# Kernel tuning notes

Measured on AMD Instinct MI355X. Metric: run time of the kernel, lower is better.

Reference implementation:

```python
import jax, jax.numpy as jnp
import numpy as np
import math

S, B, L, D = 4096, 2048, 256, 128  # substructure pool, batch, max substructs/drug, hidden


def setup_inputs() -> dict:
    key = jax.random.key(0)
    ks = jax.random.split(key, 6)
    sub_feat = jax.random.normal(ks[0], (S, D), dtype=jnp.float32)
    sub_index = jax.random.randint(ks[1], (B, L), 0, S)
    # ragged lengths -> padded prefix mask (1.0 = valid substructure)
    lengths = jax.random.randint(ks[2], (B,), 8, L + 1)
    mask = (jnp.arange(L)[None, :] < lengths[:, None]).astype(jnp.float32)
    scale = 1.0 / math.sqrt(D)
    Wq = jax.random.normal(ks[3], (D, D), dtype=jnp.float32) * scale
    Wk = jax.random.normal(ks[4], (D, D), dtype=jnp.float32) * scale
    bq = jnp.zeros((D,), dtype=jnp.float32)
    bk = jnp.zeros((D,), dtype=jnp.float32)
    return {"sub_feat": sub_feat, "mask": mask, "Wq": Wq, "bq": bq,
            "Wk": Wk, "bk": bk, "sub_index": sub_index}


def reference(sub_feat, mask, Wq, bq, Wk, bk, sub_index):
    # per-drug gather of substructure ('expert') features: [B, L, D]
    gathered = sub_feat[sub_index]
    # single-head Q/K projections (V is computed but unused in the original)
    q = gathered @ Wq + bq  # [B, L, D]
    k = gathered @ Wk + bk  # [B, L, D]
    inv_sqrt_d = 1.0 / math.sqrt(D)
    # additive mask: (1 - m) * -10000 broadcast over query dim
    add_mask = (1.0 - mask)[:, None, :] * -10000.0  # [B, 1, L]
    scores = jnp.einsum('bid,bjd->bij', q, k) * inv_sqrt_d + add_mask  # [B, L, L]
    probs = jax.nn.softmax(scores, axis=-1)
    # O[:, 0, 0, :] in the original: head 0, query position 0
    score = probs[:, 0, :]  # [B, L]
    # drug_feat[i] = score[i] @ sub_feat[sub_index[i]]
    drug_embeddings = jnp.einsum('bl,bld->bd', score, gathered)  # [B, D]
    return drug_embeddings
```

## Files before the change

### kernel.cpp

```cpp
#include <hip/hip_runtime.h>

#define DIM 128
#define LEN 256
#define INV_SQRT_D 0.08838834764831845f

#define WS_MT   0
#define WS_C    (DIM * DIM)
#define WS_W2   (DIM * DIM + DIM)
#define WS_BQBK (DIM * DIM + 2 * DIM)

__global__ __launch_bounds__(128) void precompute_kernel(
    const float* __restrict__ Wq, const float* __restrict__ bq,
    const float* __restrict__ Wk, const float* __restrict__ bk,
    float* __restrict__ ws)
{
    const int t = threadIdx.x;
    const int j = blockIdx.x;
    if (j < DIM) {
        __shared__ float wqj[DIM];
        wqj[t] = Wq[j * DIM + t];
        __syncthreads();
        const float4* row = reinterpret_cast<const float4*>(Wk + t * DIM);
        float acc = 0.f;
        #pragma unroll 8
        for (int i = 0; i < DIM / 4; ++i) {
            float4 u = row[i];
            acc = fmaf(u.x, wqj[4*i+0], acc);
            acc = fmaf(u.y, wqj[4*i+1], acc);
            acc = fmaf(u.z, wqj[4*i+2], acc);
            acc = fmaf(u.w, wqj[4*i+3], acc);
        }
        ws[WS_MT + j * DIM + t] = acc;
    } else {
        __shared__ float bqs[DIM], bks[DIM], red[DIM];
        bqs[t] = bq[t]; bks[t] = bk[t];
        __syncthreads();
        const float4* rk = reinterpret_cast<const float4*>(Wk + t * DIM);
        const float4* rq = reinterpret_cast<const float4*>(Wq + t * DIM);
        float accC = 0.f, accW = 0.f;
        #pragma unroll 8
        for (int i = 0; i < DIM / 4; ++i) {
            float4 a  = rk[i];
            float4 b2 = rq[i];
            accC = fmaf(a.x,  bqs[4*i+0], accC);
            accC = fmaf(a.y,  bqs[4*i+1], accC);
            accC = fmaf(a.z,  bqs[4*i+2], accC);
            accC = fmaf(a.w,  bqs[4*i+3], accC);
            accW = fmaf(b2.x, bks[4*i+0], accW);
            accW = fmaf(b2.y, bks[4*i+1], accW);
            accW = fmaf(b2.z, bks[4*i+2], accW);
            accW = fmaf(b2.w, bks[4*i+3], accW);
        }
        ws[WS_C  + t] = accC;
        ws[WS_W2 + t] = accW;
        red[t] = bqs[t] * bks[t];
        __syncthreads();
        if (t == 0) {
            float s = 0.f;
            for (int i = 0; i < DIM; ++i) s += red[i];
            ws[WS_BQBK] = s;
        }
    }
}

__global__ __launch_bounds__(256) void fused_kernel(
    const float* __restrict__ sub_feat, const float* __restrict__ mask,
    const int* __restrict__ sub_index, const float* __restrict__ ws,
    float* __restrict__ out)
{
    const int t    = threadIdx.x;
    const int lane = t & 63;
    const int wv   = t >> 6;
    const int pair = wv >> 1;
    const int rhalf= wv & 1;
    const int b    = blockIdx.x * 2 + pair;
    const int c32  = lane & 31;
    const int h    = lane >> 5;
    const int g    = lane >> 4;
    const int m16  = lane & 15;

    const float* Mt = ws + WS_MT;
    const float* cc = ws + WS_C;
    const float* w2 = ws + WS_W2;

    __shared__ float g0s [4][DIM];
    __shared__ int   idxs[4][DIM];
    __shared__ float bias[4][DIM];
    __shared__ float OW  [4][DIM];
    __shared__ float mzw [4][2];

    float* g0w = g0s[wv];
    int*   idw = idxs[wv];
    float* bw  = bias[wv];

    const int*   ib = sub_index + (size_t)b * LEN + rhalf * DIM;
    const float* mb = mask      + (size_t)b * LEN + rhalf * DIM;

    idw[lane]      = ib[lane];
    idw[lane + 64] = ib[lane + 64];
    bw[lane]       = (1.f - mb[lane])      * (-10000.f);
    bw[lane + 64]  = (1.f - mb[lane + 64]) * (-10000.f);

    const int r0 = sub_index[(size_t)b * LEN];
    const float2 g0p = reinterpret_cast<const float2*>(sub_feat + (size_t)r0 * DIM)[lane];
    g0w[2 * lane]     = g0p.x;
    g0w[2 * lane + 1] = g0p.y;

    float qp = g0p.x * w2[2 * lane] + g0p.y * w2[2 * lane + 1];
    #pragma unroll
    for (int o = 32; o > 0; o >>= 1) qp += __shfl_xor(qp, o);
    const float q0bk = qp + ws[WS_BQBK];

    float4 vacc = make_float4(0.f, 0.f, 0.f, 0.f);
    {
        const int jb = h * 64;
        #pragma unroll 8
        for (int k = 0; k < 64; ++k) {
            const int j = jb + k;
            const float gg = g0w[j];
            const float4 u = reinterpret_cast<const float4*>(Mt + j * DIM)[c32];
            vacc.x = fmaf(gg, u.x, vacc.x);
            vacc.y = fmaf(gg, u.y, vacc.y);
            vacc.z = fmaf(gg, u.z, vacc.z);
            vacc.w = fmaf(gg, u.w, vacc.w);
        }
    }
    vacc.x += __shfl_xor(vacc.x, 32);
    vacc.y += __shfl_xor(vacc.y, 32);
    vacc.z += __shfl_xor(vacc.z, 32);
    vacc.w += __shfl_xor(vacc.w, 32);
    const float4 cv = reinterpret_cast<const float4*>(cc)[c32];
    float4 vt;
    vt.x = vacc.x + cv.x; vt.y = vacc.y + cv.y;
    vt.z = vacc.z + cv.z; vt.w = vacc.w + cv.w;

    float4 vA, vB;
    vA.x = __shfl(vt.x, m16);      vA.y = __shfl(vt.y, m16);
    vA.z = __shfl(vt.z, m16);      vA.w = __shfl(vt.w, m16);
    vB.x = __shfl(vt.x, m16 + 16); vB.y = __shfl(vt.y, m16 + 16);
    vB.z = __shfl(vt.z, m16 + 16); vB.w = __shfl(vt.w, m16 + 16);

    float mx = -1e30f, Zr = 0.f;
    float O0=0.f,O1=0.f,O2=0.f,O3=0.f,O4=0.f,O5=0.f,O6=0.f,O7=0.f;
    #pragma unroll 4
    for (int k = 0; k < 32; ++k) {
        const int jl = 4 * k + g;
        const int ij = idw[jl];
        const float bj = bw[jl];
        const float* rp = sub_feat + (size_t)ij * DIM + 4 * m16;
        const float4 u0 = *reinterpret_cast<const float4*>(rp);
        const float4 u1 = *reinterpret_cast<const float4*>(rp + 64);
        float sd = u0.x*vA.x + u0.y*vA.y + u0.z*vA.z + u0.w*vA.w
                 + u1.x*vB.x + u1.y*vB.y + u1.z*vB.z + u1.w*vB.w;
        sd += __shfl_xor(sd, 1);
        sd += __shfl_xor(sd, 2);
        sd += __shfl_xor(sd, 4);
        sd += __shfl_xor(sd, 8);
        const float s  = (sd + q0bk) * INV_SQRT_D + bj;
        const float mn = fmaxf(mx, s);
        const float sc = __expf(mx - mn);
        const float e  = __expf(s - mn);
        Zr = Zr * sc + e;
        O0 = O0*sc + e*u0.x; O1 = O1*sc + e*u0.y;
        O2 = O2*sc + e*u0.z; O3 = O3*sc + e*u0.w;
        O4 = O4*sc + e*u1.x; O5 = O5*sc + e*u1.y;
        O6 = O6*sc + e*u1.z; O7 = O7*sc + e*u1.w;
        mx = mn;
    }

    #pragma unroll
    for (int msk = 16; msk <= 32; msk <<= 1) {
        const float om = __shfl_xor(mx, msk);
        const float oZ = __shfl_xor(Zr, msk);
        const float M  = fmaxf(mx, om);
        const float a  = __expf(mx - M);
        const float bb = __expf(om - M);
        float p0 = __shfl_xor(O0, msk), p1 = __shfl_xor(O1, msk);
        float p2 = __shfl_xor(O2, msk), p3 = __shfl_xor(O3, msk);
        float p4 = __shfl_xor(O4, msk), p5 = __shfl_xor(O5, msk);
        float p6 = __shfl_xor(O6, msk), p7 = __shfl_xor(O7, msk);
        Zr = a*Zr + bb*oZ;
        O0 = a*O0 + bb*p0; O1 = a*O1 + bb*p1;
        O2 = a*O2 + bb*p2; O3 = a*O3 + bb*p3;
        O4 = a*O4 + bb*p4; O5 = a*O5 + bb*p5;
        O6 = a*O6 + bb*p6; O7 = a*O7 + bb*p7;
        mx = M;
    }

    if (lane < 16) {
        reinterpret_cast<float4*>(&OW[wv][0])[m16]  = make_float4(O0, O1, O2, O3);
        reinterpret_cast<float4*>(&OW[wv][64])[m16] = make_float4(O4, O5, O6, O7);
    }
    if (lane == 0) { mzw[wv][0] = mx; mzw[wv][1] = Zr; }
    __syncthreads();

    {
        const int p = t >> 7;
        const int d = t & (DIM - 1);
        const float mA = mzw[2*p][0],   ZA = mzw[2*p][1];
        const float mB = mzw[2*p+1][0], ZB = mzw[2*p+1][1];
        const float M  = fmaxf(mA, mB);
        const float sA = __expf(mA - M);
        const float sB = __expf(mB - M);
        const float Zt = sA * ZA + sB * ZB;
        const float val = (sA * OW[2*p][d] + sB * OW[2*p+1][d]) / Zt;
        out[((size_t)blockIdx.x * 2 + p) * DIM + d] = val;
    }
}

extern "C" void kernel_launch(void* const* d_in, const int* in_sizes, int n_in,
                              void* d_out, int out_size, void* d_ws, size_t ws_size,
                              hipStream_t stream) {
    const float* sub_feat  = (const float*)d_in[0];
    const float* mask      = (const float*)d_in[1];
    const float* Wq        = (const float*)d_in[2];
    const float* bq        = (const float*)d_in[3];
    const float* Wk        = (const float*)d_in[4];
    const float* bk        = (const float*)d_in[5];
    const int*   sub_index = (const int*)d_in[6];
    float* outp = (float*)d_out;
    float* ws   = (float*)d_ws;

    const int B = in_sizes[6] / LEN;

    precompute_kernel<<<dim3(DIM + 1), dim3(DIM), 0, stream>>>(Wq, bq, Wk, bk, ws);
    fused_kernel<<<dim3(B / 2), dim3(256), 0, stream>>>(sub_feat, mask, sub_index, ws, outp);
}
```

Baseline: 31.40 us.

## Split per-drug query vector into separate kernel and drop online-softmax max tracking

Moves the per-drug projection of the query-0 vector through the folded Wq·Wk^T matrix into its own kernel. That kernel stages the 64KB matrix in shared memory and writes the vectors to workspace, and the attention kernel then just loads them. The online softmax max/rescale is replaced by a plain exp2 accumulation with log2e folded into the scale and the mask bias, which removes the per-step rescale and the max merge. This adds a kernel launch and a workspace round-trip. Without max subtraction, exp could overflow if scores are large, so it relies on the score range staying bounded.

```diff
diff --git a/kernel.cpp b/kernel.cpp
--- a/kernel.cpp
+++ b/kernel.cpp
@@ -3,11 +3,14 @@
 #define DIM 128
 #define LEN 256
 #define INV_SQRT_D 0.08838834764831845f
+#define LOG2E 1.4426950408889634f
+#define SCALE_L2 (INV_SQRT_D * LOG2E)
 
 #define WS_MT   0
 #define WS_C    (DIM * DIM)
 #define WS_W2   (DIM * DIM + DIM)
 #define WS_BQBK (DIM * DIM + 2 * DIM)
+#define WS_VBUF (DIM * DIM + 2 * DIM + 8)
 
 __global__ __launch_bounds__(128) void precompute_kernel(
     const float* __restrict__ Wq, const float* __restrict__ bq,
@@ -63,7 +66,140 @@
     }
 }
 
-__global__ __launch_bounds__(256) void fused_kernel(
+__global__ __launch_bounds__(256) void vcompute_kernel(
+    const float* __restrict__ sub_feat, const int* __restrict__ sub_index,
+    const float* __restrict__ ws, float* __restrict__ vout,
+    float* __restrict__ qout, int B)
+{
+    const int t    = threadIdx.x;
+    const int lane = t & 63;
+    const int wv   = t >> 6;
+
+    __shared__ float MtL[DIM * DIM];
+    __shared__ float g0L[4][DIM];
+
+    const float4* Msrc = reinterpret_cast<const float4*>(ws + WS_MT);
+    float4* Mdst = reinterpret_cast<float4*>(MtL);
+    #pragma unroll
+    for (int i = 0; i < 16; ++i) Mdst[t + 256 * i] = Msrc[t + 256 * i];
+    __syncthreads();
+
+    const float* w2 = ws + WS_W2;
+    const float* cc = ws + WS_C;
+    const float  bqbk = ws[WS_BQBK];
+
+    #pragma unroll
+    for (int s = 0; s < 2; ++s) {
+        const int b = blockIdx.x * 8 + wv * 2 + s;
+        if (b >= B) break;
+        const int r0 = sub_index[(size_t)b * LEN];
+        const float2 g0p = reinterpret_cast<const float2*>(sub_feat + (size_t)r0 * DIM)[lane];
+        g0L[wv][2 * lane]     = g0p.x;
+        g0L[wv][2 * lane + 1] = g0p.y;
+
+        float qp = g0p.x * w2[2 * lane] + g0p.y * w2[2 * lane + 1];
+        #pragma unroll
+        for (int o = 32; o > 0; o >>= 1) qp += __shfl_xor(qp, o);
+        if (lane == 0) qout[b] = qp + bqbk;
+
+        float a0 = 0.f, a1 = 0.f;
+        #pragma unroll 8
+        for (int j = 0; j < DIM; ++j) {
+            const float g = g0L[wv][j];
+            a0 = fmaf(g, MtL[j * DIM + lane],      a0);
+            a1 = fmaf(g, MtL[j * DIM + lane + 64], a1);
+        }
+        vout[(size_t)b * DIM + lane]      = a0 + cc[lane];
+        vout[(size_t)b * DIM + lane + 64] = a1 + cc[lane + 64];
+    }
+}
+
+__global__ __launch_bounds__(256) void attn_kernel(
+    const float* __restrict__ sub_feat, const float* __restrict__ mask,
+    const int* __restrict__ sub_index, const float* __restrict__ vbuf,
+    const float* __restrict__ qbuf, float* __restrict__ out, int B)
+{
+    const int t    = threadIdx.x;
+    const int lane = t & 63;
+    const int wv   = t >> 6;
+    const int pair = wv >> 1;
+    const int rhalf= wv & 1;
+    const int b    = blockIdx.x * 2 + pair;
+    const int g    = lane >> 4;
+    const int m16  = lane & 15;
+
+    __shared__ int   idxs[4][DIM];
+    __shared__ float bias[4][DIM];
+    __shared__ float OW  [4][DIM];
+    __shared__ float Zw  [4];
+
+    float Zr = 0.f;
+    float O0=0.f,O1=0.f,O2=0.f,O3=0.f,O4=0.f,O5=0.f,O6=0.f,O7=0.f;
+
+    if (b < B) {
+        int*   idw = idxs[wv];
+        float* bw  = bias[wv];
+        const int*   ib = sub_index + (size_t)b * LEN + rhalf * DIM;
+        const float* mb = mask      + (size_t)b * LEN + rhalf * DIM;
+        idw[lane]      = ib[lane];
+        idw[lane + 64] = ib[lane + 64];
+        bw[lane]       = (1.f - mb[lane])      * (-10000.f * LOG2E);
+        bw[lane + 64]  = (1.f - mb[lane + 64]) * (-10000.f * LOG2E);
+
+        const float4 vA = reinterpret_cast<const float4*>(vbuf + (size_t)b * DIM)[m16];
+        const float4 vB = reinterpret_cast<const float4*>(vbuf + (size_t)b * DIM)[m16 + 16];
+        const float qterm = qbuf[b] * SCALE_L2;
+
+        #pragma unroll 4
+        for (int k = 0; k < 32; ++k) {
+            const int jl = 4 * k + g;
+            const int ij = idw[jl];
+            const float bj = bw[jl];
+            const float* rp = sub_feat + (size_t)ij * DIM + 4 * m16;
+            const float4 u0 = *reinterpret_cast<const float4*>(rp);
+            const float4 u1 = *reinterpret_cast<const float4*>(rp + 64);
+            float sd = u0.x*vA.x + u0.y*vA.y + u0.z*vA.z + u0.w*vA.w
+                     + u1.x*vB.x + u1.y*vB.y + u1.z*vB.z + u1.w*vB.w;
+            sd += __shfl_xor(sd, 1);
+            sd += __shfl_xor(sd, 2);
+            sd += __shfl_xor(sd, 4);
+            sd += __shfl_xor(sd, 8);
+            const float e = exp2f(sd * SCALE_L2 + qterm + bj);
+            Zr += e;
+            O0 = fmaf(e, u0.x, O0); O1 = fmaf(e, u0.y, O1);
+            O2 = fmaf(e, u0.z, O2); O3 = fmaf(e, u0.w, O3);
+            O4 = fmaf(e, u1.x, O4); O5 = fmaf(e, u1.y, O5);
+            O6 = fmaf(e, u1.z, O6); O7 = fmaf(e, u1.w, O7);
+        }
+
+        #pragma unroll
+        for (int msk = 16; msk <= 32; msk <<= 1) {
+            Zr += __shfl_xor(Zr, msk);
+            O0 += __shfl_xor(O0, msk); O1 += __shfl_xor(O1, msk);
+            O2 += __shfl_xor(O2, msk); O3 += __shfl_xor(O3, msk);
+            O4 += __shfl_xor(O4, msk); O5 += __shfl_xor(O5, msk);
+            O6 += __shfl_xor(O6, msk); O7 += __shfl_xor(O7, msk);
+        }
+        if (lane < 16) {
+            reinterpret_cast<float4*>(&OW[wv][0])[m16]  = make_float4(O0, O1, O2, O3);
+            reinterpret_cast<float4*>(&OW[wv][64])[m16] = make_float4(O4, O5, O6, O7);
+        }
+        if (lane == 0) Zw[wv] = Zr;
+    }
+    __syncthreads();
+
+    {
+        const int p = t >> 7;
+        const int d = t & (DIM - 1);
+        const int ob = blockIdx.x * 2 + p;
+        if (ob < B) {
+            const float Zt = Zw[2*p] + Zw[2*p+1];
+            out[(size_t)ob * DIM + d] = (OW[2*p][d] + OW[2*p+1][d]) / Zt;
+        }
+    }
+}
+
+__global__ __launch_bounds__(256) void fused_fallback(
     const float* __restrict__ sub_feat, const float* __restrict__ mask,
     const int* __restrict__ sub_index, const float* __restrict__ ws,
     float* __restrict__ out)
@@ -87,7 +223,7 @@
     __shared__ int   idxs[4][DIM];
     __shared__ float bias[4][DIM];
     __shared__ float OW  [4][DIM];
-    __shared__ float mzw [4][2];
+    __shared__ float Zw  [4];
 
     float* g0w = g0s[wv];
     int*   idw = idxs[wv];
@@ -95,11 +231,10 @@
 
     const int*   ib = sub_index + (size_t)b * LEN + rhalf * DIM;
     const float* mb = mask      + (size_t)b * LEN + rhalf * DIM;
-
     idw[lane]      = ib[lane];
     idw[lane + 64] = ib[lane + 64];
-    bw[lane]       = (1.f - mb[lane])      * (-10000.f);
-    bw[lane + 64]  = (1.f - mb[lane + 64]) * (-10000.f);
+    bw[lane]       = (1.f - mb[lane])      * (-10000.f * LOG2E);
+    bw[lane + 64]  = (1.f - mb[lane + 64]) * (-10000.f * LOG2E);
 
     const int r0 = sub_index[(size_t)b * LEN];
     const float2 g0p = reinterpret_cast<const float2*>(sub_feat + (size_t)r0 * DIM)[lane];
@@ -109,7 +244,7 @@
     float qp = g0p.x * w2[2 * lane] + g0p.y * w2[2 * lane + 1];
     #pragma unroll
     for (int o = 32; o > 0; o >>= 1) qp += __shfl_xor(qp, o);
-    const float q0bk = qp + ws[WS_BQBK];
+    const float qterm = (qp + ws[WS_BQBK]) * SCALE_L2;
 
     float4 vacc = make_float4(0.f, 0.f, 0.f, 0.f);
     {
@@ -140,7 +275,7 @@
     vB.x = __shfl(vt.x, m16 + 16); vB.y = __shfl(vt.y, m16 + 16);
     vB.z = __shfl(vt.z, m16 + 16); vB.w = __shfl(vt.w, m16 + 16);
 
-    float mx = -1e30f, Zr = 0.f;
+    float Zr = 0.f;
     float O0=0.f,O1=0.f,O2=0.f,O3=0.f,O4=0.f,O5=0.f,O6=0.f,O7=0.f;
     #pragma unroll 4
     for (int k = 0; k < 32; ++k) {
@@ -156,55 +291,33 @@
         sd += __shfl_xor(sd, 2);
         sd += __shfl_xor(sd, 4);
         sd += __shfl_xor(sd, 8);
-        const float s  = (sd + q0bk) * INV_SQRT_D + bj;
-        const float mn = fmaxf(mx, s);
-        const float sc = __expf(mx - mn);
-        const float e  = __expf(s - mn);
-        Zr = Zr * sc + e;
-        O0 = O0*sc + e*u0.x; O1 = O1*sc + e*u0.y;
-        O2 = O2*sc + e*u0.z; O3 = O3*sc + e*u0.w;
-        O4 = O4*sc + e*u1.x; O5 = O5*sc + e*u1.y;
-        O6 = O6*sc + e*u1.z; O7 = O7*sc + e*u1.w;
-        mx = mn;
-    }
-
+        const float e = exp2f(sd * SCALE_L2 + qterm + bj);
+        Zr += e;
+        O0 = fmaf(e, u0.x, O0); O1 = fmaf(e, u0.y, O1);
+        O2 = fmaf(e, u0.z, O2); O3 = fmaf(e, u0.w, O3);
+        O4 = fmaf(e, u1.x, O4); O5 = fmaf(e, u1.y, O5);
+        O6 = fmaf(e, u1.z, O6); O7 = fmaf(e, u1.w, O7);
+    }
     #pragma unroll
     for (int msk = 16; msk <= 32; msk <<= 1) {
-        const float om = __shfl_xor(mx, msk);
-        const float oZ = __shfl_xor(Zr, msk);
-        const float M  = fmaxf(mx, om);
-        const float a  = __expf(mx - M);
-        const float bb = __expf(om - M);
-        float p0 = __shfl_xor(O0, msk), p1 = __shfl_xor(O1, msk);
-        float p2 = __shfl_xor(O2, msk), p3 = __shfl_xor(O3, msk);
-        float p4 = __shfl_xor(O4, msk), p5 = __shfl_xor(O5, msk);
-        float p6 = __shfl_xor(O6, msk), p7 = __shfl_xor(O7, msk);
-        Zr = a*Zr + bb*oZ;
-        O0 = a*O0 + bb*p0; O1 = a*O1 + bb*p1;
-        O2 = a*O2 + bb*p2; O3 = a*O3 + bb*p3;
-        O4 = a*O4 + bb*p4; O5 = a*O5 + bb*p5;
-        O6 = a*O6 + bb*p6; O7 = a*O7 + bb*p7;
-        mx = M;
-    }
-
+        Zr += __shfl_xor(Zr, msk);
+        O0 += __shfl_xor(O0, msk); O1 += __shfl_xor(O1, msk);
+        O2 += __shfl_xor(O2, msk); O3 += __shfl_xor(O3, msk);
+        O4 += __shfl_xor(O4, msk); O5 += __shfl_xor(O5, msk);
+        O6 += __shfl_xor(O6, msk); O7 += __shfl_xor(O7, msk);
+    }
     if (lane < 16) {
         reinterpret_cast<float4*>(&OW[wv][0])[m16]  = make_float4(O0, O1, O2, O3);
         reinterpret_cast<float4*>(&OW[wv][64])[m16] = make_float4(O4, O5, O6, O7);
     }
-    if (lane == 0) { mzw[wv][0] = mx; mzw[wv][1] = Zr; }
+    if (lane == 0) Zw[wv] = Zr;
     __syncthreads();
 
     {
         const int p = t >> 7;
         const int d = t & (DIM - 1);
-        const float mA = mzw[2*p][0],   ZA = mzw[2*p][1];
-        const float mB = mzw[2*p+1][0], ZB = mzw[2*p+1][1];
-        const float M  = fmaxf(mA, mB);
-        const float sA = __expf(mA - M);
-        const float sB = __expf(mB - M);
-        const float Zt = sA * ZA + sB * ZB;
-        const float val = (sA * OW[2*p][d] + sB * OW[2*p+1][d]) / Zt;
-        out[((size_t)blockIdx.x * 2 + p) * DIM + d] = val;
+        const float Zt = Zw[2*p] + Zw[2*p+1];
+        out[((size_t)blockIdx.x * 2 + p) * DIM + d] = (OW[2*p][d] + OW[2*p+1][d]) / Zt;
     }
 }
 
@@ -222,7 +335,19 @@
     float* ws   = (float*)d_ws;
 
     const int B = in_sizes[6] / LEN;
+    const size_t needed = ((size_t)WS_VBUF + (size_t)B * DIM + (size_t)B) * sizeof(float);
 
     precompute_kernel<<<dim3(DIM + 1), dim3(DIM), 0, stream>>>(Wq, bq, Wk, bk, ws);
-    fused_kernel<<<dim3(B / 2), dim3(256), 0, stream>>>(sub_feat, mask, sub_index, ws, outp);
-}
+
+    if (ws_size >= needed) {
+        float* vbuf = ws + WS_VBUF;
+        float* qbuf = vbuf + (size_t)B * DIM;
+        vcompute_kernel<<<dim3((B + 7) / 8), dim3(256), 0, stream>>>(
+            sub_feat, sub_index, ws, vbuf, qbuf, B);
+        attn_kernel<<<dim3((B + 1) / 2), dim3(256), 0, stream>>>(
+            sub_feat, mask, sub_index, vbuf, qbuf, outp, B);
+    } else {
+        fused_fallback<<<dim3(B / 2), dim3(256), 0, stream>>>(
+            sub_feat, mask, sub_index, ws, outp);
+    }
+}
```

Result: slower. 32.47 us (+3.4%).
